# Optimization experiments

Measured on AMD Instinct MI355X. Metric: run time of the kernel, lower is better.

The kernel has to match this reference:

```python
import jax, jax.numpy as jnp
import numpy as np

B, T, IN, H, OUT = 1024, 512, 16, 64, 8


def setup_inputs() -> dict:
    key = jax.random.key(0)
    ks = jax.random.split(key, 7)
    s = 1.0 / np.sqrt(H)
    return {
        "x": jax.random.normal(ks[0], (B, T, IN), dtype=jnp.float32),
        "W_ih": jax.random.normal(ks[1], (4 * H, IN), dtype=jnp.float32) * s,
        "W_hh": jax.random.normal(ks[2], (4 * H, H), dtype=jnp.float32) * s,
        "b_ih": jax.random.normal(ks[3], (4 * H,), dtype=jnp.float32) * s,
        "b_hh": jax.random.normal(ks[4], (4 * H,), dtype=jnp.float32) * s,
        "W_fc": jax.random.normal(ks[5], (OUT, H), dtype=jnp.float32) * s,
        "b_fc": jax.random.normal(ks[6], (OUT,), dtype=jnp.float32) * s,
    }


def reference(x, W_ih, W_hh, b_ih, b_hh, W_fc, b_fc):
    Bq, Tq, _ = x.shape
    Hq = W_hh.shape[1]
    # Precompute input contribution for all timesteps: [T, B, 4H]
    xw = jnp.einsum("bti,gi->tbg", x, W_ih) + b_ih + b_hh

    def step(carry, xw_t):
        h, c = carry
        gates = xw_t + h @ W_hh.T  # [B, 4H]
        i, f, g, o = jnp.split(gates, 4, axis=-1)  # PyTorch gate order i,f,g,o
        i = jax.nn.sigmoid(i)
        f = jax.nn.sigmoid(f)
        g = jnp.tanh(g)
        o = jax.nn.sigmoid(o)
        c = f * c + i * g
        h = o * jnp.tanh(c)
        return (h, c), None

    h0 = jnp.zeros((Bq, Hq), dtype=x.dtype)
    c0 = jnp.zeros((Bq, Hq), dtype=x.dtype)
    (h_last, _), _ = jax.lax.scan(step, (h0, c0), xw)

    # fc on last timestep only, then sigmoid -> [B, 1, OUT]
    out = jax.nn.sigmoid(h_last @ W_fc.T + b_fc)
    return out[:, None, :]
```

## Files before the change

kernel.cpp:

```cpp
#include <hip/hip_runtime.h>
#include <math.h>


#define LSTM_T 512
#define LSTM_IN 16
#define LSTM_H 64
#define LSTM_OUT 8
#define BT 2
#define HSTRIDE 80
#define HPSTR 320
#define XSTR 73
#define XWSZ 2336

#define L2E   1.44269504088896340736f
#define L2E2  2.88539008177792681472f

typedef _Float16 half8  __attribute__((ext_vector_type(8)));
typedef float    floatx4 __attribute__((ext_vector_type(4)));

static __device__ __forceinline__ float fast_rcp(float x) { return __builtin_amdgcn_rcpf(x); }
static __device__ __forceinline__ float fast_exp2(float x) { return __builtin_amdgcn_exp2f(x); }
static __device__ __forceinline__ float sigm2(float p) { return fast_rcp(1.0f + fast_exp2(-p)); }
static __device__ __forceinline__ void pin4(int4& v) {
    asm volatile("" : "+v"(v.x), "+v"(v.y), "+v"(v.z), "+v"(v.w));
}
static __device__ __forceinline__ void pinf4(float4& v) {
    asm volatile("" : "+v"(v.x), "+v"(v.y), "+v"(v.z), "+v"(v.w));
}
static __device__ __forceinline__ void lite_barrier() {
    asm volatile("s_waitcnt lgkmcnt(0)\n\ts_barrier" ::: "memory");
}
static __device__ __forceinline__ unsigned pk2h(float a, float b) {
    return __builtin_bit_cast(unsigned, __builtin_amdgcn_cvt_pkrtz(a, b));
}
static __device__ __forceinline__ half8 to_h8(float4 a, float4 b) {
    uint4 u = make_uint4(pk2h(a.x, a.y), pk2h(a.z, a.w), pk2h(b.x, b.y), pk2h(b.z, b.w));
    return __builtin_bit_cast(half8, u);
}
static __device__ __forceinline__ int4 cvt8h(float4 a, float4 b) {
    return __builtin_bit_cast(int4, to_h8(a, b));
}
static __device__ __forceinline__ float4 ld4(const float* p) {
    return *reinterpret_cast<const float4*>(p);
}
static __device__ __forceinline__ float4 scl4(float4 v, float s) {
    return make_float4(s * v.x, s * v.y, s * v.z, s * v.w);
}
static __device__ __forceinline__ float sel4(floatx4 v, bool r0, bool r1) {
    float lo = r0 ? v[1] : v[0];
    float hi = r0 ? v[3] : v[2];
    return r1 ? hi : lo;
}
static __device__ __forceinline__ float dpp8(float v) {
    int r = __builtin_amdgcn_update_dpp(0, __builtin_bit_cast(int, v),
                                        0x128, 0xF, 0xF, false);
    return __builtin_bit_cast(float, r);
}

#define MF(A_, B_, C_) __builtin_amdgcn_mfma_f32_16x16x32_f16( \
        __builtin_bit_cast(half8, A_), (B_), (C_), 0, 0, 0)
#define B4(i) __builtin_bit_cast(floatx4, bias4[i])

__global__ __launch_bounds__(256, 2)
void lstm_mfma_kernel(const float* __restrict__ x,
                      const float* __restrict__ W_ih,
                      const float* __restrict__ W_hh,
                      const float* __restrict__ b_ih,
                      const float* __restrict__ b_hh,
                      const float* __restrict__ W_fc,
                      const float* __restrict__ b_fc,
                      float* __restrict__ out) {
    const int tid   = threadIdx.x;
    const int lane  = tid & 63;
    const int w     = tid >> 6;
    const int q     = lane >> 4;
    const int m     = lane & 15;
    const int b     = m & 1;
    const int dt    = m >> 1;
    const int rho   = (m >> 1) & 3;
    const bool r0   = (rho & 1) != 0;
    const bool r1   = (rho & 2) != 0;
    const bool h1   = (m & 8) != 0;
    const int h1i   = h1 ? 1 : 0;
    const bool wr   = (m < 8);
    const int jmine = 16 * w + 4 * q + rho;
    const int bbase = blockIdx.x * BT;

    const float a1 = h1 ? L2E2 : 0.0f;
    const float b1 = h1 ? (-2.0f * L2E2) : 1.0f;

    __shared__ __align__(16)  float2   xwbuf[2][XWSZ];
    __shared__ __align__(128) _Float16 hbuf[2][2 * BT][HSTRIDE];
    __shared__ __align__(16)  float    hfin[BT][LSTM_H];

    int4 Ah[4][2], Ax[4];
    float4 bias4[4];
    #pragma unroll
    for (int tt = 0; tt < 4; ++tt) {
        const float sc = (tt == 2) ? L2E2 : -L2E;
        const int gt = tt * 64 + 16 * w + m;
        #pragma unroll
        for (int c = 0; c < 2; ++c) {
            const float* s = W_hh + gt * LSTM_H + 32 * c + 8 * q;
            Ah[tt][c] = cvt8h(scl4(ld4(s), sc), scl4(ld4(s + 4), sc));
            pin4(Ah[tt][c]);
        }
        float4 xa = make_float4(0.f, 0.f, 0.f, 0.f), xb = xa;
        if (q < 2) {
            const float* s = W_ih + gt * LSTM_IN + 8 * q;
            xa = ld4(s); xb = ld4(s + 4);
        }
        Ax[tt] = cvt8h(scl4(xa, sc), scl4(xb, sc));
        pin4(Ax[tt]);
        const int gb = tt * 64 + 16 * w + 4 * q;
        float4 bi = ld4(b_ih + gb), bh = ld4(b_hh + gb);
        bias4[tt] = make_float4(sc * (bi.x + bh.x), sc * (bi.y + bh.y),
                                sc * (bi.z + bh.z), sc * (bi.w + bh.w));
        pinf4(bias4[tt]);
    }

    float4 zc4 = make_float4(0.f, 0.f, 0.f, 0.f);
    pinf4(zc4);
    const floatx4 zc = __builtin_bit_cast(floatx4, zc4);

    const float2* xwp[8];
    #pragma unroll
    for (int k = 0; k < 8; ++k)
        xwp[k] = &xwbuf[0][(2 * b + h1i) * XSTR + (jmine ^ k)];
    float2* xww[2][4];
    #pragma unroll
    for (int pr = 0; pr < 2; ++pr)
        #pragma unroll
        for (int r = 0; r < 4; ++r)
            xww[pr][r] = &xwbuf[0][(dt * 4 + 2 * b + pr) * XSTR
                                   + ((16 * w + 4 * q + r) ^ dt)];
    const _Float16* hrp = &hbuf[0][b][8 * q];
    _Float16*       hwp = &hbuf[0][h1 ? 2 + b : b][jmine];

    if (tid < 160) reinterpret_cast<int*>(&hbuf[0][0][0])[tid] = 0;

    const float* xpb = x + (size_t)(bbase + b) * LSTM_T * LSTM_IN
                         + (size_t)dt * LSTM_IN + 8 * q;
    float4 Xb0 = make_float4(0.f, 0.f, 0.f, 0.f), Xb1 = Xb0;
    if (q < 2) { Xb0 = ld4(xpb); Xb1 = ld4(xpb + 4); }

#define BWR(WB, PR, R_)                                                         \
    xww[PR][R_][(WB) * XWSZ] = (PR)                                             \
        ? make_float2(aXg_[R_], aXo_[R_])                                       \
        : make_float2(aXf_[R_], aXi_[R_]);                                      \
    xww[PR][(R_) + 1][(WB) * XWSZ] = (PR)                                       \
        ? make_float2(aXg_[(R_) + 1], aXo_[(R_) + 1])                           \
        : make_float2(aXf_[(R_) + 1], aXi_[(R_) + 1]);

    floatx4 aXi_, aXf_, aXg_, aXo_;
    half8 xfb;
    {
        half8 x0 = to_h8(Xb0, Xb1);
        aXi_ = MF(Ax[0], x0, B4(0));
        aXf_ = MF(Ax[1], x0, B4(1));
        aXg_ = MF(Ax[2], x0, B4(2));
        aXo_ = MF(Ax[3], x0, B4(3));
        BWR(0, 0, 0) BWR(0, 0, 2) BWR(0, 1, 0) BWR(0, 1, 2)
    }
    if (q < 2) {
        Xb0 = ld4(xpb + 8 * LSTM_IN);
        Xb1 = ld4(xpb + 8 * LSTM_IN + 4);
    }
    __syncthreads();

    float2 xwc = xwp[0][0];
    float cs = 0.0f, hreg = 0.0f;

#define STEP_CORE(PK, KN, NC, ...)                                              \
    {                                                                           \
        half8 bh0 = *reinterpret_cast<const half8*>(hrp + (PK) * HPSTR);        \
        half8 bh1 = *reinterpret_cast<const half8*>(hrp + (PK) * HPSTR + 32);   \
        __VA_ARGS__                                                             \
                               \
        float2 xwn = xwp[KN][(NC) * XWSZ + (KN) * 4 * XSTR];                    \
                       \
        floatx4 accf = MF(Ah[1][0], bh0, zc);                                   \
        floatx4 accg = MF(Ah[2][0], bh0, zc);                                   \
        floatx4 acci = MF(Ah[0][0], bh0, zc);                                   \
        floatx4 acco = MF(Ah[3][0], bh0, zc);                                   \
        accf = MF(Ah[1][1], bh1, accf);                                         \
        accg = MF(Ah[2][1], bh1, accg);                                         \
        __builtin_amdgcn_s_setprio(1);                                          \
        float uf = sel4(accf, r0, r1);                                          \
        float ug = sel4(accg, r0, r1);                                          \
        float u1 = (h1 ? ug : uf) + xwc.x;                                      \
        float e1 = fast_exp2(u1);                                               \
        acci = MF(Ah[0][1], bh1, acci);                                         \
        acco = MF(Ah[3][1], bh1, acco);                                         \
                            \
        float act1 = fmaf(b1, fast_rcp(1.0f + e1), a1);                         \
        float uii = sel4(acci, r0, r1);                                         \
        float uoo = sel4(acco, r0, r1);                                         \
        float u2 = (h1 ? uoo : uii) + xwc.y;                                    \
        float e2 = fast_exp2(u2);                                               \
        float act2 = fast_rcp(1.0f + e2);         \
        float g_in = dpp8(act1);                      \
        float o_in = dpp8(act2);                          \
                \
        cs = fmaf(act1, cs, act2 * g_in);                                       \
        float E  = fast_exp2(cs);                                               \
        float r_ = fast_rcp(1.0f + E);                                          \
        float n2o = -2.0f * o_in;                        \
        hreg = fmaf(n2o, r_, o_in);                           \
        hwp[((PK) ^ 1) * HPSTR] = (_Float16)hreg;            \
        __builtin_amdgcn_s_setprio(0);                                          \
        lite_barrier();                                                         \
        xwc = xwn;                                                              \
    }

    for (int t16 = 0; t16 < LSTM_T; t16 += 16) {
        const bool more = (t16 + 16) < LSTM_T;
        STEP_CORE(0, 1, 0,
            { xfb = to_h8(Xb0, Xb1); aXi_ = MF(Ax[0], xfb, B4(0)); })
        STEP_CORE(1, 2, 0, { aXf_ = MF(Ax[1], xfb, B4(1)); })
        STEP_CORE(0, 3, 0, { aXg_ = MF(Ax[2], xfb, B4(2)); })
        STEP_CORE(1, 4, 0, { aXo_ = MF(Ax[3], xfb, B4(3)); })
        STEP_CORE(0, 5, 0, { BWR(1, 0, 0) })
        STEP_CORE(1, 6, 0, { BWR(1, 0, 2) })
        STEP_CORE(0, 7, 0, { BWR(1, 1, 0)
            if (q < 2 && more) Xb0 = ld4(xpb + (size_t)(t16 + 16) * LSTM_IN); })
        STEP_CORE(1, 0, 1, { BWR(1, 1, 2)
            if (q < 2 && more) Xb1 = ld4(xpb + (size_t)(t16 + 16) * LSTM_IN + 4); })
        STEP_CORE(0, 1, 1,
            { if (more) { xfb = to_h8(Xb0, Xb1); aXi_ = MF(Ax[0], xfb, B4(0)); } })
        STEP_CORE(1, 2, 1, { if (more) { aXf_ = MF(Ax[1], xfb, B4(1)); } })
        STEP_CORE(0, 3, 1, { if (more) { aXg_ = MF(Ax[2], xfb, B4(2)); } })
        STEP_CORE(1, 4, 1, { if (more) { aXo_ = MF(Ax[3], xfb, B4(3)); } })
        STEP_CORE(0, 5, 1, { if (more) { BWR(0, 0, 0) } })
        STEP_CORE(1, 6, 1, { if (more) { BWR(0, 0, 2) } })
        STEP_CORE(0, 7, 1, { if (more) { BWR(0, 1, 0) }
            if (q < 2 && more) Xb0 = ld4(xpb + (size_t)(t16 + 24) * LSTM_IN); })
        STEP_CORE(1, 0, 0, { if (more) { BWR(0, 1, 2) }
            if (q < 2 && more) Xb1 = ld4(xpb + (size_t)(t16 + 24) * LSTM_IN + 4); })
    }
#undef STEP_CORE
#undef BWR

    if (wr) hfin[b][jmine] = hreg;
    __syncthreads();

    if (tid < BT * LSTM_OUT) {
        int bb = tid >> 3, o = tid & 7;
        float s = b_fc[o];
        #pragma unroll
        for (int j4 = 0; j4 < LSTM_H / 4; ++j4) {
            float4 wv = ld4(W_fc + o * LSTM_H + 4 * j4);
            float4 hv = *reinterpret_cast<const float4*>(&hfin[bb][4 * j4]);
            s = fmaf(wv.x, hv.x, s);
            s = fmaf(wv.y, hv.y, s);
            s = fmaf(wv.z, hv.z, s);
            s = fmaf(wv.w, hv.w, s);
        }
        out[(size_t)(bbase + bb) * LSTM_OUT + o] = sigm2(s * L2E);
    }
}

extern "C" void kernel_launch(void* const* d_in, const int* in_sizes, int n_in,
                              void* d_out, int out_size, void* d_ws, size_t ws_size,
                              hipStream_t stream) {
    const float* x    = (const float*)d_in[0];
    const float* W_ih = (const float*)d_in[1];
    const float* W_hh = (const float*)d_in[2];
    const float* b_ih = (const float*)d_in[3];
    const float* b_hh = (const float*)d_in[4];
    const float* W_fc = (const float*)d_in[5];
    const float* b_fc = (const float*)d_in[6];
    float* out = (float*)d_out;

    lstm_mfma_kernel<<<1024 / BT, 256, 0, stream>>>(
        x, W_ih, W_hh, b_ih, b_hh, W_fc, b_fc, out);
}
```

Baseline: 222.2 us.

## Split LSTM gate work across 8 waves with 4 batch rows per block

Each workgroup now runs 4 sequences with 512 threads (8 waves), so each wave computes 8 hidden units for two fused gate pairs (f/g and i/o) using 4 MFMAs per step instead of 8. The cross-lane exchange of the g and o activations moves from DPP to ds_swizzle, and the input projection is prefetched every 4 steps in place of 8, with a new xw buffer layout. This shortens the serial per-step MFMA chain, which is the latency-bound recurrence, at the cost of a wider barrier across 8 waves, half as many blocks, and an LDS-based swizzle.

```diff
diff --git a/kernel.cpp b/kernel.cpp
--- a/kernel.cpp
+++ b/kernel.cpp
@@ -6,11 +6,11 @@
 #define LSTM_IN 16
 #define LSTM_H 64
 #define LSTM_OUT 8
-#define BT 2
+#define BT 4
 #define HSTRIDE 80
-#define HPSTR 320
-#define XSTR 73
-#define XWSZ 2336
+#define HPSTR 640
+#define XSTR 67
+#define XWSZ 2144
 
 #define L2E   1.44269504088896340736f
 #define L2E2  2.88539008177792681472f
@@ -51,17 +51,15 @@
     float hi = r0 ? v[3] : v[2];
     return r1 ? hi : lo;
 }
-static __device__ __forceinline__ float dpp8(float v) {
-    int r = __builtin_amdgcn_update_dpp(0, __builtin_bit_cast(int, v),
-                                        0x128, 0xF, 0xF, false);
+static __device__ __forceinline__ float swz16(float v) {
+    int r = __builtin_amdgcn_ds_swizzle(__builtin_bit_cast(int, v), 0x401F);
     return __builtin_bit_cast(float, r);
 }
 
 #define MF(A_, B_, C_) __builtin_amdgcn_mfma_f32_16x16x32_f16( \
         __builtin_bit_cast(half8, A_), (B_), (C_), 0, 0, 0)
-#define B4(i) __builtin_bit_cast(floatx4, bias4[i])
-
-__global__ __launch_bounds__(256, 2)
+
+__global__ __launch_bounds__(512, 2)
 void lstm_mfma_kernel(const float* __restrict__ x,
                       const float* __restrict__ W_ih,
                       const float* __restrict__ W_hh,
@@ -75,173 +73,158 @@
     const int w     = tid >> 6;
     const int q     = lane >> 4;
     const int m     = lane & 15;
-    const int b     = m & 1;
-    const int dt    = m >> 1;
-    const int rho   = (m >> 1) & 3;
+    const int b     = m & 3;
+    const int rho   = m >> 2;
     const bool r0   = (rho & 1) != 0;
     const bool r1   = (rho & 2) != 0;
-    const bool h1   = (m & 8) != 0;
-    const int h1i   = h1 ? 1 : 0;
-    const bool wr   = (m < 8);
-    const int jmine = 16 * w + 4 * q + rho;
+    const int gh    = q & 1;
+    const int jj    = q >> 1;
+    const int jmine = 8 * w + 4 * jj + rho;
     const int bbase = blockIdx.x * BT;
 
-    const float a1 = h1 ? L2E2 : 0.0f;
-    const float b1 = h1 ? (-2.0f * L2E2) : 1.0f;
+    const float a1 = gh ? L2E2 : 0.0f;
+    const float b1 = gh ? (-2.0f * L2E2) : 1.0f;
 
     __shared__ __align__(16)  float2   xwbuf[2][XWSZ];
     __shared__ __align__(128) _Float16 hbuf[2][2 * BT][HSTRIDE];
     __shared__ __align__(16)  float    hfin[BT][LSTM_H];
 
-    int4 Ah[4][2], Ax[4];
-    float4 bias4[4];
+    const int  ghr = (m >> 2) & 1;
+    const int  jl  = 4 * (m >> 3) + (m & 3);
+    const int  gFG = ghr ? 2 : 1;
+    const int  gIO = ghr ? 3 : 0;
+    const float sFG = ghr ? L2E2 : -L2E;
+    const int growFG = gFG * 64 + 8 * w + jl;
+    const int growIO = gIO * 64 + 8 * w + jl;
+    int4 AhFG[2], AhIO[2], AxFG, AxIO;
     #pragma unroll
-    for (int tt = 0; tt < 4; ++tt) {
-        const float sc = (tt == 2) ? L2E2 : -L2E;
-        const int gt = tt * 64 + 16 * w + m;
-        #pragma unroll
-        for (int c = 0; c < 2; ++c) {
-            const float* s = W_hh + gt * LSTM_H + 32 * c + 8 * q;
-            Ah[tt][c] = cvt8h(scl4(ld4(s), sc), scl4(ld4(s + 4), sc));
-            pin4(Ah[tt][c]);
+    for (int c = 0; c < 2; ++c) {
+        const float* s1 = W_hh + growFG * LSTM_H + 32 * c + 8 * q;
+        AhFG[c] = cvt8h(scl4(ld4(s1), sFG), scl4(ld4(s1 + 4), sFG));
+        pin4(AhFG[c]);
+        const float* s2 = W_hh + growIO * LSTM_H + 32 * c + 8 * q;
+        AhIO[c] = cvt8h(scl4(ld4(s2), -L2E), scl4(ld4(s2 + 4), -L2E));
+        pin4(AhIO[c]);
+    }
+    {
+        float4 za = make_float4(0.f, 0.f, 0.f, 0.f), zb = za;
+        float4 xa = za, xb = za, ya = za, yb = za;
+        if (q < 2) {
+            const float* s1 = W_ih + growFG * LSTM_IN + 8 * q;
+            xa = ld4(s1); xb = ld4(s1 + 4);
+            const float* s2 = W_ih + growIO * LSTM_IN + 8 * q;
+            ya = ld4(s2); yb = ld4(s2 + 4);
         }
-        float4 xa = make_float4(0.f, 0.f, 0.f, 0.f), xb = xa;
-        if (q < 2) {
-            const float* s = W_ih + gt * LSTM_IN + 8 * q;
-            xa = ld4(s); xb = ld4(s + 4);
-        }
-        Ax[tt] = cvt8h(scl4(xa, sc), scl4(xb, sc));
-        pin4(Ax[tt]);
-        const int gb = tt * 64 + 16 * w + 4 * q;
-        float4 bi = ld4(b_ih + gb), bh = ld4(b_hh + gb);
-        bias4[tt] = make_float4(sc * (bi.x + bh.x), sc * (bi.y + bh.y),
-                                sc * (bi.z + bh.z), sc * (bi.w + bh.w));
-        pinf4(bias4[tt]);
-    }
+        AxFG = cvt8h(scl4(xa, sFG), scl4(xb, sFG));  pin4(AxFG);
+        AxIO = cvt8h(scl4(ya, -L2E), scl4(yb, -L2E)); pin4(AxIO);
+        (void)za; (void)zb;
+    }
+    float4 bFG4, bIO4;
+    {
+        const float scq = (q & 1) ? L2E2 : -L2E;
+        const int gb1 = ((q & 1) ? 2 : 1) * 64 + 8 * w + 4 * (q >> 1);
+        float4 bi = ld4(b_ih + gb1), bh = ld4(b_hh + gb1);
+        bFG4 = make_float4(scq * (bi.x + bh.x), scq * (bi.y + bh.y),
+                           scq * (bi.z + bh.z), scq * (bi.w + bh.w));
+        pinf4(bFG4);
+        const int gb2 = ((q & 1) ? 3 : 0) * 64 + 8 * w + 4 * (q >> 1);
+        float4 ci = ld4(b_ih + gb2), ch = ld4(b_hh + gb2);
+        bIO4 = make_float4(-L2E * (ci.x + ch.x), -L2E * (ci.y + ch.y),
+                           -L2E * (ci.z + ch.z), -L2E * (ci.w + ch.w));
+        pinf4(bIO4);
+    }
+    const floatx4 bFGv = __builtin_bit_cast(floatx4, bFG4);
+    const floatx4 bIOv = __builtin_bit_cast(floatx4, bIO4);
 
     float4 zc4 = make_float4(0.f, 0.f, 0.f, 0.f);
     pinf4(zc4);
     const floatx4 zc = __builtin_bit_cast(floatx4, zc4);
 
-    const float2* xwp[8];
-    #pragma unroll
-    for (int k = 0; k < 8; ++k)
-        xwp[k] = &xwbuf[0][(2 * b + h1i) * XSTR + (jmine ^ k)];
-    float2* xww[2][4];
-    #pragma unroll
-    for (int pr = 0; pr < 2; ++pr)
-        #pragma unroll
-        for (int r = 0; r < 4; ++r)
-            xww[pr][r] = &xwbuf[0][(dt * 4 + 2 * b + pr) * XSTR
-                                   + ((16 * w + 4 * q + r) ^ dt)];
+    const float2* xwr = &xwbuf[0][(b * 2 + gh) * XSTR + jmine];
+    float2*       xww = &xwbuf[0][(8 * (m >> 2) + 2 * (m & 3) + (q & 1)) * XSTR
+                                  + 8 * w + 4 * (q >> 1)];
     const _Float16* hrp = &hbuf[0][b][8 * q];
-    _Float16*       hwp = &hbuf[0][h1 ? 2 + b : b][jmine];
-
-    if (tid < 160) reinterpret_cast<int*>(&hbuf[0][0][0])[tid] = 0;
+    _Float16*       hwp = &hbuf[0][gh ? 4 + b : b][jmine];
+
+    if (tid < 320) reinterpret_cast<int*>(&hbuf[0][0][0])[tid] = 0;
 
     const float* xpb = x + (size_t)(bbase + b) * LSTM_T * LSTM_IN
-                         + (size_t)dt * LSTM_IN + 8 * q;
+                         + (size_t)(m >> 2) * LSTM_IN + 8 * q;
     float4 Xb0 = make_float4(0.f, 0.f, 0.f, 0.f), Xb1 = Xb0;
     if (q < 2) { Xb0 = ld4(xpb); Xb1 = ld4(xpb + 4); }
 
-#define BWR(WB, PR, R_)                                                         \
-    xww[PR][R_][(WB) * XWSZ] = (PR)                                             \
-        ? make_float2(aXg_[R_], aXo_[R_])                                       \
-        : make_float2(aXf_[R_], aXi_[R_]);                                      \
-    xww[PR][(R_) + 1][(WB) * XWSZ] = (PR)                                       \
-        ? make_float2(aXg_[(R_) + 1], aXo_[(R_) + 1])                           \
-        : make_float2(aXf_[(R_) + 1], aXi_[(R_) + 1]);
-
-    floatx4 aXi_, aXf_, aXg_, aXo_;
+#define WX(BUF, P_) xww[(BUF) * XWSZ + (P_)] = make_float2(aFGx[P_], aIOx[P_]);
+
+    floatx4 aFGx, aIOx;
     half8 xfb;
     {
         half8 x0 = to_h8(Xb0, Xb1);
-        aXi_ = MF(Ax[0], x0, B4(0));
-        aXf_ = MF(Ax[1], x0, B4(1));
-        aXg_ = MF(Ax[2], x0, B4(2));
-        aXo_ = MF(Ax[3], x0, B4(3));
-        BWR(0, 0, 0) BWR(0, 0, 2) BWR(0, 1, 0) BWR(0, 1, 2)
+        aFGx = MF(AxFG, x0, bFGv);
+        aIOx = MF(AxIO, x0, bIOv);
+        WX(0, 0) WX(0, 1) WX(0, 2) WX(0, 3)
     }
     if (q < 2) {
-        Xb0 = ld4(xpb + 8 * LSTM_IN);
-        Xb1 = ld4(xpb + 8 * LSTM_IN + 4);
+        Xb0 = ld4(xpb + 4 * LSTM_IN);
+        Xb1 = ld4(xpb + 4 * LSTM_IN + 4);
     }
     __syncthreads();
 
-    float2 xwc = xwp[0][0];
+    float2 xwc = xwr[0];
     float cs = 0.0f, hreg = 0.0f;
 
-#define STEP_CORE(PK, KN, NC, ...)                                              \
+#define STEP_CORE(PK, KN, NCB, ...)                                             \
     {                                                                           \
         half8 bh0 = *reinterpret_cast<const half8*>(hrp + (PK) * HPSTR);        \
         half8 bh1 = *reinterpret_cast<const half8*>(hrp + (PK) * HPSTR + 32);   \
         __VA_ARGS__                                                             \
-                               \
-        float2 xwn = xwp[KN][(NC) * XWSZ + (KN) * 4 * XSTR];                    \
-                       \
-        floatx4 accf = MF(Ah[1][0], bh0, zc);                                   \
-        floatx4 accg = MF(Ah[2][0], bh0, zc);                                   \
-        floatx4 acci = MF(Ah[0][0], bh0, zc);                                   \
-        floatx4 acco = MF(Ah[3][0], bh0, zc);                                   \
-        accf = MF(Ah[1][1], bh1, accf);                                         \
-        accg = MF(Ah[2][1], bh1, accg);                                         \
+        float2 xwn = xwr[(NCB) * XWSZ + (KN) * 8 * XSTR];                       \
+        floatx4 accFG = MF(AhFG[0], bh0, zc);                                   \
+        floatx4 accIO = MF(AhIO[0], bh0, zc);                                   \
+        accFG = MF(AhFG[1], bh1, accFG);                                        \
+        accIO = MF(AhIO[1], bh1, accIO);                                        \
         __builtin_amdgcn_s_setprio(1);                                          \
-        float uf = sel4(accf, r0, r1);                                          \
-        float ug = sel4(accg, r0, r1);                                          \
-        float u1 = (h1 ? ug : uf) + xwc.x;                                      \
+        float u1 = sel4(accFG, r0, r1) + xwc.x;                                 \
         float e1 = fast_exp2(u1);                                               \
-        acci = MF(Ah[0][1], bh1, acci);                                         \
-        acco = MF(Ah[3][1], bh1, acco);                                         \
-                            \
+        float u2 = sel4(accIO, r0, r1) + xwc.y;                                 \
         float act1 = fmaf(b1, fast_rcp(1.0f + e1), a1);                         \
-        float uii = sel4(acci, r0, r1);                                         \
-        float uoo = sel4(acco, r0, r1);                                         \
-        float u2 = (h1 ? uoo : uii) + xwc.y;                                    \
         float e2 = fast_exp2(u2);                                               \
-        float act2 = fast_rcp(1.0f + e2);         \
-        float g_in = dpp8(act1);                      \
-        float o_in = dpp8(act2);                          \
-                \
+        float act2 = fast_rcp(1.0f + e2);                                       \
+        float g_in = swz16(act1);                    \
+        float o_in = swz16(act2);                        \
         cs = fmaf(act1, cs, act2 * g_in);                                       \
         float E  = fast_exp2(cs);                                               \
         float r_ = fast_rcp(1.0f + E);                                          \
-        float n2o = -2.0f * o_in;                        \
-        hreg = fmaf(n2o, r_, o_in);                           \
-        hwp[((PK) ^ 1) * HPSTR] = (_Float16)hreg;            \
+        float n2o = -2.0f * o_in;                                               \
+        hreg = fmaf(n2o, r_, o_in);                            \
+        hwp[((PK) ^ 1) * HPSTR] = (_Float16)hreg;         \
         __builtin_amdgcn_s_setprio(0);                                          \
         lite_barrier();                                                         \
         xwc = xwn;                                                              \
     }
 
-    for (int t16 = 0; t16 < LSTM_T; t16 += 16) {
-        const bool more = (t16 + 16) < LSTM_T;
+    for (int t8 = 0; t8 < LSTM_T; t8 += 8) {
+        const bool mA = t8 + 4  < LSTM_T;
+        const bool mB = t8 + 8  < LSTM_T;
+        const bool xB = t8 + 12 < LSTM_T;
         STEP_CORE(0, 1, 0,
-            { xfb = to_h8(Xb0, Xb1); aXi_ = MF(Ax[0], xfb, B4(0)); })
-        STEP_CORE(1, 2, 0, { aXf_ = MF(Ax[1], xfb, B4(1)); })
-        STEP_CORE(0, 3, 0, { aXg_ = MF(Ax[2], xfb, B4(2)); })
-        STEP_CORE(1, 4, 0, { aXo_ = MF(Ax[3], xfb, B4(3)); })
-        STEP_CORE(0, 5, 0, { BWR(1, 0, 0) })
-        STEP_CORE(1, 6, 0, { BWR(1, 0, 2) })
-        STEP_CORE(0, 7, 0, { BWR(1, 1, 0)
-            if (q < 2 && more) Xb0 = ld4(xpb + (size_t)(t16 + 16) * LSTM_IN); })
-        STEP_CORE(1, 0, 1, { BWR(1, 1, 2)
-            if (q < 2 && more) Xb1 = ld4(xpb + (size_t)(t16 + 16) * LSTM_IN + 4); })
+            { if (mA) { xfb = to_h8(Xb0, Xb1); aFGx = MF(AxFG, xfb, bFGv); } })
+        STEP_CORE(1, 2, 0, { if (mA) { aIOx = MF(AxIO, xfb, bIOv); } })
+        STEP_CORE(0, 3, 0, { if (mA) { WX(1, 0) WX(1, 1) } })
+        STEP_CORE(1, 0, 1, { if (mA) { WX(1, 2) WX(1, 3) }
+            if (q < 2 && mB) { Xb0 = ld4(xpb + (size_t)(t8 + 8) * LSTM_IN);
+                               Xb1 = ld4(xpb + (size_t)(t8 + 8) * LSTM_IN + 4); } })
         STEP_CORE(0, 1, 1,
-            { if (more) { xfb = to_h8(Xb0, Xb1); aXi_ = MF(Ax[0], xfb, B4(0)); } })
-        STEP_CORE(1, 2, 1, { if (more) { aXf_ = MF(Ax[1], xfb, B4(1)); } })
-        STEP_CORE(0, 3, 1, { if (more) { aXg_ = MF(Ax[2], xfb, B4(2)); } })
-        STEP_CORE(1, 4, 1, { if (more) { aXo_ = MF(Ax[3], xfb, B4(3)); } })
-        STEP_CORE(0, 5, 1, { if (more) { BWR(0, 0, 0) } })
-        STEP_CORE(1, 6, 1, { if (more) { BWR(0, 0, 2) } })
-        STEP_CORE(0, 7, 1, { if (more) { BWR(0, 1, 0) }
-            if (q < 2 && more) Xb0 = ld4(xpb + (size_t)(t16 + 24) * LSTM_IN); })
-        STEP_CORE(1, 0, 0, { if (more) { BWR(0, 1, 2) }
-            if (q < 2 && more) Xb1 = ld4(xpb + (size_t)(t16 + 24) * LSTM_IN + 4); })
+            { if (mB) { xfb = to_h8(Xb0, Xb1); aFGx = MF(AxFG, xfb, bFGv); } })
+        STEP_CORE(1, 2, 1, { if (mB) { aIOx = MF(AxIO, xfb, bIOv); } })
+        STEP_CORE(0, 3, 1, { if (mB) { WX(0, 0) WX(0, 1) } })
+        STEP_CORE(1, 0, 0, { if (mB) { WX(0, 2) WX(0, 3) }
+            if (q < 2 && xB) { Xb0 = ld4(xpb + (size_t)(t8 + 12) * LSTM_IN);
+                               Xb1 = ld4(xpb + (size_t)(t8 + 12) * LSTM_IN + 4); } })
     }
 #undef STEP_CORE
-#undef BWR
-
-    if (wr) hfin[b][jmine] = hreg;
+#undef WX
+
+    if (!gh) hfin[b][jmine] = hreg;
     __syncthreads();
 
     if (tid < BT * LSTM_OUT) {
@@ -272,6 +255,6 @@
     const float* b_fc = (const float*)d_in[6];
     float* out = (float*)d_out;
 
-    lstm_mfma_kernel<<<1024 / BT, 256, 0, stream>>>(
+    lstm_mfma_kernel<<<1024 / BT, 512, 0, stream>>>(
         x, W_ih, W_hh, b_ih, b_hh, W_fc, b_fc, out);
 }
```

Result: slower. 237.3 us (+6.8%).
